# Optimization experiments

Measured on AMD Instinct MI355X. Metric: run time of the kernel, lower is better.

The kernel has to match this reference:

```python
import jax, jax.numpy as jnp
import numpy as np

DELAY_TAPS = np.array([1, 4, 24, 96, 168])
MAX_DELAY = int(DELAY_TAPS.max())
LEAK_RATE = 0.1
RESERVOIR_DIM = 256
INPUT_DIM = 1
N_TAPS = len(DELAY_TAPS)
TARGET_RADIUS = 0.95


def setup_inputs() -> dict:
    key = jax.random.key(0)
    kx, kin, kfb, kb = jax.random.split(key, 4)
    B, T = 64, 2048
    x = jax.random.normal(kx, (B, T, INPUT_DIM), dtype=jnp.float32)
    # W_in ~ U(-0.5, 0.5)
    W_in = jax.random.uniform(kin, (RESERVOIR_DIM, INPUT_DIM), dtype=jnp.float32,
                              minval=-0.5, maxval=0.5)
    # W_fb: sparse gaussian rescaled to ~per-tap spectral radius
    per_tap_radius = TARGET_RADIUS / np.sqrt(N_TAPS)
    kfb1, kfb2 = jax.random.split(kfb)
    W = jax.random.normal(kfb1, (N_TAPS, RESERVOIR_DIM, RESERVOIR_DIM), dtype=jnp.float32)
    mask = jax.random.uniform(kfb2, W.shape) < 0.1
    W = W * mask
    # approx spectral radius of sparse gaussian ~ sqrt(R * density)
    approx_radius = np.sqrt(RESERVOIR_DIM * 0.1)
    W_fb = W * (per_tap_radius / approx_radius)
    tap_weights = jnp.ones((N_TAPS,), dtype=jnp.float32)
    bias = jax.random.uniform(kb, (RESERVOIR_DIM,), dtype=jnp.float32,
                              minval=-0.1, maxval=0.1)
    return {"x": x, "W_in": W_in, "W_fb": W_fb,
            "tap_weights": tap_weights, "bias": bias}


def reference(x, W_in, W_fb, tap_weights, bias):
    B, T, _ = x.shape
    R = W_in.shape[0]
    # static gather positions into rolling history buffer of length MAX_DELAY
    # history[:, -1] holds state at t-1  ->  state at t - tau lives at MAX_DELAY - tau
    pos = MAX_DELAY - DELAY_TAPS  # numpy, static

    drive = jnp.einsum('bti,ri->btr', x, W_in)  # (B,T,R)
    tap_w = jax.nn.softmax(tap_weights)

    h0 = jnp.zeros((B, R), x.dtype)
    hist0 = jnp.zeros((B, MAX_DELAY, R), x.dtype)

    def step(carry, d_t):
        h, hist = carry
        delayed = hist[:, pos, :]  # (B,K,R)
        fb = jnp.einsum('k,bkr,krs->bs', tap_w, delayed, W_fb)
        h_new = (1.0 - LEAK_RATE) * h + LEAK_RATE * jnp.tanh(d_t + fb + bias)
        hist = jnp.concatenate([hist[:, 1:], h_new[:, None, :]], axis=1)
        return (h_new, hist), h_new

    drive_t = jnp.swapaxes(drive, 0, 1)  # (T,B,R)
    _, states = jax.lax.scan(step, (h0, hist0), drive_t)
    return jnp.swapaxes(states, 0, 1)  # (B,T,R)
```

## Files before the change

### kernel.cpp

```cpp
#include <hip/hip_runtime.h>
#include <math.h>

typedef __attribute__((ext_vector_type(8))) short bf16x8;
typedef __attribute__((ext_vector_type(4))) float f32x4;

#define BB 64
#define TT 2048
#define RR 256
#define BLK 24
#define NTHR 512
#define HB_PAD 776
#define HW_PAD 288

#define MFMA(a, b, c) __builtin_amdgcn_mfma_f32_16x16x32_bf16((a), (b), (c), 0, 0, 0)

__device__ __forceinline__ unsigned short f2bf(float f) {
    unsigned u = __float_as_uint(f);
    return (unsigned short)((u + 0x7FFFu + ((u >> 16) & 1u)) >> 16);
}
__device__ __forceinline__ float bf2f(unsigned short h) {
    return __uint_as_float(((unsigned)h) << 16);
}
__device__ __forceinline__ float fast_tanh(float x) {
    float e = __expf(2.0f * x);
    return 1.0f - 2.0f * __builtin_amdgcn_rcpf(1.0f + e);
}

__global__ void pack_weights(const float* __restrict__ W_fb,
                             const float* __restrict__ tapw,
                             unsigned short* __restrict__ bp) {
    int gid = blockIdx.x * 256 + threadIdx.x;
    int l = gid & 63, c = gid >> 6;
    int tap = c >> 7;
    int rem = c & 127;
    int kt = rem >> 4, nt = rem & 15;

    float v0 = tapw[0], v1 = tapw[1], v2 = tapw[2], v3 = tapw[3], v4 = tapw[4];
    float mx = fmaxf(fmaxf(fmaxf(v0, v1), fmaxf(v2, v3)), v4);
    float e0 = expf(v0 - mx), e1 = expf(v1 - mx), e2 = expf(v2 - mx),
          e3 = expf(v3 - mx), e4 = expf(v4 - mx);
    float inv = 1.0f / (e0 + e1 + e2 + e3 + e4);
    float tws[5] = {e0 * inv, e1 * inv, e2 * inv, e3 * inv, e4 * inv};
    float tw = tws[tap];

    int kbase = 32 * kt + 8 * (l >> 4);
    int n = 16 * nt + (l & 15);
    const float* W = W_fb + tap * 65536;
    unsigned short t[8];
#pragma unroll
    for (int j = 0; j < 8; ++j) t[j] = f2bf(tw * W[(kbase + j) * 256 + n]);
    uint4 o;
    o.x = (unsigned)t[0] | ((unsigned)t[1] << 16);
    o.y = (unsigned)t[2] | ((unsigned)t[3] << 16);
    o.z = (unsigned)t[4] | ((unsigned)t[5] << 16);
    o.w = (unsigned)t[6] | ((unsigned)t[7] << 16);
    *(uint4*)(bp + (size_t)(c * 64 + l) * 8) = o;
}

__global__ __launch_bounds__(NTHR, 1)
void reservoir_mfma(const float* __restrict__ x,
                    const float* __restrict__ W_in,
                    const float* __restrict__ bias,
                    const unsigned short* __restrict__ bp,
                    float* __restrict__ out)
{
    const int b    = blockIdx.x;
    const int tid  = threadIdx.x;
    const int lane = tid & 63;
    const int w    = tid >> 6;
    const int l15  = lane & 15;
    const int quad = lane >> 4;

    __shared__ float xs[TT];
    __shared__ unsigned short hwinb[8][2][HW_PAD];
    __shared__ unsigned short hbcb[BLK][2][HB_PAD];
    __shared__ float2 Gl2[BLK][130];
    __shared__ float hob[BLK][RR];

    for (int i = tid; i < TT; i += NTHR) xs[i] = x[b * TT + i];
    {
        unsigned* hz = (unsigned*)&hwinb[0][0][0];
        for (int i = tid; i < 8 * 2 * HW_PAD / 2; i += NTHR) hz[i] = 0u;
    }

    const bf16x8* bpv = (const bf16x8*)bp;
    bf16x8 b1[8][2], b4[8][2];
#pragma unroll
    for (int kt = 0; kt < 8; ++kt)
#pragma unroll
        for (int u = 0; u < 2; ++u) {
            int nt = 2 * w + u;
            b1[kt][u] = bpv[((0 * 8 + kt) * 16 + nt) * 64 + lane];
            b4[kt][u] = bpv[((1 * 8 + kt) * 16 + nt) * 64 + lane];
        }

    const int s0g = 32 * w + l15, s1g = s0g + 16;
    const float win0 = W_in[s0g], win1 = W_in[s1g];
    const float bi0 = bias[s0g], bi1 = bias[s1g];
    float hp0 = 0.0f, hp1 = 0.0f;

    const float* outr = out + (size_t)b * TT * RR;
    float*       outw = out + (size_t)b * TT * RR;

    const unsigned short* hw1v = &hwinb[0][l15 & 1][0];
    const unsigned short* hw4v = &hwinb[0][(l15 >> 2) & 1][0];
    const unsigned short* fa1  = &hbcb[16 + (l15 & 7)][(l15 >> 3) & 1][0];
    const size_t HWSLOT = 2 * HW_PAD;

    const int varw  = quad >> 1;
    const int s_w   = 32 * w + l15 + ((quad & 1) << 4);
    unsigned short* const hwb = &hwinb[0][0][0];
    const unsigned hw_off = (unsigned)(varw * HW_PAD + s_w);

    __syncthreads();

    for (int t0 = 0; t0 < TT; t0 += BLK) {
#pragma unroll
        for (int it = 0; it < 9; ++it) {
            int i = it * NTHR + tid;
            int j = i / 192;
            int p = i - j * 192;
            int r = 4 * p;
            int kf = r >> 8, rr = r & 255;
            float4 v = {0.f, 0.f, 0.f, 0.f};
            if (kf == 0) {
                if (t0 > 0) v = *(const float4*)&hob[j][rr];
            } else {
                int dk = (kf == 1) ? 96 : 168;
                int tt = t0 + j - dk;
                if (tt >= 0) v = *(const float4*)(outr + (size_t)tt * RR + rr);
            }
            unsigned short h0 = f2bf(v.x), h1 = f2bf(v.y), h2 = f2bf(v.z), h3 = f2bf(v.w);
            unsigned short q0 = f2bf(v.x - bf2f(h0)), q1 = f2bf(v.y - bf2f(h1)),
                           q2 = f2bf(v.z - bf2f(h2)), q3 = f2bf(v.w - bf2f(h3));
            uint2 H = { (unsigned)h0 | ((unsigned)h1 << 16), (unsigned)h2 | ((unsigned)h3 << 16) };
            uint2 Q = { (unsigned)q0 | ((unsigned)q1 << 16), (unsigned)q2 | ((unsigned)q3 << 16) };
            *(uint2*)&hbcb[j][0][r] = H;
            *(uint2*)&hbcb[j][1][r] = Q;
        }
        __syncthreads();

        f32x4 zf = {0.f, 0.f, 0.f, 0.f};
        f32x4 cf00a = zf, cf01a = zf, cf00b = zf, cf01b = zf, cf10 = zf, cf11 = zf;
        const int r0a = l15;
        const int cw0 = 2 * w, cw1 = 2 * w + 1;
        bf16x8 p0A = bpv[((16 + 0) * 16 + cw0) * 64 + lane];
        bf16x8 p0B = bpv[((16 + 0) * 16 + cw1) * 64 + lane];
        bf16x8 p1A = bpv[((16 + 1) * 16 + cw0) * 64 + lane];
        bf16x8 p1B = bpv[((16 + 1) * 16 + cw1) * 64 + lane];
        bf16x8 p2A = bpv[((16 + 2) * 16 + cw0) * 64 + lane];
        bf16x8 p2B = bpv[((16 + 2) * 16 + cw1) * 64 + lane];
#pragma unroll 1
        for (int g = 0; g < 8; ++g) {
            const int base = 3 * g;
            {
                int ro = 32 * base + 8 * quad;
                bf16x8 a00 = *(const bf16x8*)&hbcb[r0a][0][ro];
                bf16x8 a01 = *(const bf16x8*)&hbcb[r0a][1][ro];
                bf16x8 a1  = *(const bf16x8*)&fa1[ro];
                cf00a = MFMA(a00, p0A, cf00a); cf01a = MFMA(a00, p0B, cf01a);
                cf00b = MFMA(a01, p0A, cf00b); cf01b = MFMA(a01, p0B, cf01b);
                cf10  = MFMA(a1,  p0A, cf10);  cf11  = MFMA(a1,  p0B, cf11);
                int nf = base + 3; if (nf > 23) nf = 23;
                p0A = bpv[((16 + nf) * 16 + cw0) * 64 + lane];
                p0B = bpv[((16 + nf) * 16 + cw1) * 64 + lane];
            }
            {
                int ro = 32 * (base + 1) + 8 * quad;
                bf16x8 a00 = *(const bf16x8*)&hbcb[r0a][0][ro];
                bf16x8 a01 = *(const bf16x8*)&hbcb[r0a][1][ro];
                bf16x8 a1  = *(const bf16x8*)&fa1[ro];
                cf00a = MFMA(a00, p1A, cf00a); cf01a = MFMA(a00, p1B, cf01a);
                cf00b = MFMA(a01, p1A, cf00b); cf01b = MFMA(a01, p1B, cf01b);
                cf10  = MFMA(a1,  p1A, cf10);  cf11  = MFMA(a1,  p1B, cf11);
                int nf = base + 4; if (nf > 23) nf = 23;
                p1A = bpv[((16 + nf) * 16 + cw0) * 64 + lane];
                p1B = bpv[((16 + nf) * 16 + cw1) * 64 + lane];
            }
            {
                int ro = 32 * (base + 2) + 8 * quad;
                bf16x8 a00 = *(const bf16x8*)&hbcb[r0a][0][ro];
                bf16x8 a01 = *(const bf16x8*)&hbcb[r0a][1][ro];
                bf16x8 a1  = *(const bf16x8*)&fa1[ro];
                cf00a = MFMA(a00, p2A, cf00a); cf01a = MFMA(a00, p2B, cf01a);
                cf00b = MFMA(a01, p2A, cf00b); cf01b = MFMA(a01, p2B, cf01b);
                cf10  = MFMA(a1,  p2A, cf10);  cf11  = MFMA(a1,  p2B, cf11);
                int nf = base + 5; if (nf > 23) nf = 23;
                p2A = bpv[((16 + nf) * 16 + cw0) * 64 + lane];
                p2B = bpv[((16 + nf) * 16 + cw1) * 64 + lane];
            }
        }
        f32x4 cf00 = cf00a + cf00b, cf01 = cf01a + cf01b;
        float cf10f[4], cf11f[4];
#pragma unroll
        for (int i = 0; i < 4; ++i) {
            cf10f[i] = cf10[i] + __shfl_xor(cf10[i], 32, 64);
            cf11f[i] = cf11[i] + __shfl_xor(cf11[i], 32, 64);
        }
#pragma unroll
        for (int i = 0; i < 4; ++i) {
            int j0 = 4 * quad + i;
            int tx0 = t0 + j0; float xv0 = xs[tx0 < TT ? tx0 : TT - 1];
            Gl2[j0][16 * w + l15] =
                make_float2(cf00[i] + bi0 + xv0 * win0, cf01[i] + bi1 + xv0 * win1);
            int j1 = 16 + 4 * quad + i;
            if (j1 < BLK) {
                int tx1 = t0 + j1; float xv1 = xs[tx1 < TT ? tx1 : TT - 1];
                Gl2[j1][16 * w + l15] =
                    make_float2(cf10f[i] + bi0 + xv1 * win0, cf11f[i] + bi1 + xv1 * win1);
            }
        }
        __syncthreads();

        const int tend = (t0 + BLK < TT) ? (t0 + BLK) : TT;
#pragma unroll 1
        for (int t4 = t0; t4 < tend; t4 += 4) {
            f32x4 c40 = zf, c41 = zf;
            const int sl = (t4 - 4 + (l15 & 3)) & 7;
            const unsigned short* hw4 = hw4v + (size_t)sl * HWSLOT;
#pragma unroll
            for (int kt = 0; kt < 8; ++kt) {
                int ro = 32 * kt + 8 * quad;
                bf16x8 a = *(const bf16x8*)&hw4[ro];
                c40 = MFMA(a, b4[kt][0], c40);
                c41 = MFMA(a, b4[kt][1], c41);
            }
            float c40f[4], c41f[4];
#pragma unroll
            for (int u2 = 0; u2 < 4; ++u2) {
                c40f[u2] = c40[u2] + __shfl_xor(c40[u2], 16, 64);
                c41f[u2] = c41[u2] + __shfl_xor(c41[u2], 16, 64);
            }
#pragma unroll
            for (int u = 0; u < 4; ++u) {
                const int t = t4 + u;
                const int sp = (t - 1) & 7;
                const unsigned short* hw1 = hw1v + (size_t)sp * HWSLOT;
                f32x4 c10 = zf, c11 = zf;
#pragma unroll
                for (int kt = 0; kt < 8; ++kt) {
                    int ro = 32 * kt + 8 * quad;
                    bf16x8 a = *(const bf16x8*)&hw1[ro];
                    c10 = MFMA(a, b1[kt][0], c10);
                    c11 = MFMA(a, b1[kt][1], c11);
                }
                const int jj = t - t0;
                const int wsl = t & 7;
                float2 gl = Gl2[jj][16 * w + l15];
                float f0 = (c10[0] + c10[1]) + c40f[u] + gl.x;
                float f1 = (c11[0] + c11[1]) + c41f[u] + gl.y;
                float h0 = 0.9f * hp0 + 0.1f * fast_tanh(f0);
                float h1 = 0.9f * hp1 + 0.1f * fast_tanh(f1);
                hp0 = h0; hp1 = h1;
                unsigned short hh0 = f2bf(h0), hh1 = f2bf(h1);
                unsigned short lo0 = f2bf(h0 - bf2f(hh0)), lo1 = f2bf(h1 - bf2f(hh1));
                unsigned short v0 = varw ? lo0 : hh0;
                unsigned short v1 = varw ? lo1 : hh1;
                unsigned short wv = (quad & 1) ? v1 : v0;
                hwb[(size_t)wsl * HWSLOT + hw_off] = wv;
                if (quad < 2) hob[jj][s_w] = (quad & 1) ? h1 : h0;
                __syncthreads();
            }
        }

        {
            const int nf4 = (tend - t0) * (RR / 4);
            const float4* src = (const float4*)&hob[0][0];
            float4* dst = (float4*)(outw + (size_t)t0 * RR);
#pragma unroll
            for (int it = 0; it < 3; ++it) {
                int idx = it * NTHR + tid;
                if (idx < nf4) dst[idx] = src[idx];
            }
        }
    }
}

extern "C" void kernel_launch(void* const* d_in, const int* in_sizes, int n_in,
                              void* d_out, int out_size, void* d_ws, size_t ws_size,
                              hipStream_t stream) {
    const float* x    = (const float*)d_in[0];
    const float* W_in = (const float*)d_in[1];
    const float* W_fb = (const float*)d_in[2];
    const float* tapw = (const float*)d_in[3];
    const float* bias = (const float*)d_in[4];
    float* out = (float*)d_out;
    unsigned short* bp = (unsigned short*)d_ws;

    pack_weights<<<160, 256, 0, stream>>>(W_fb, tapw, bp);
    reservoir_mfma<<<BB, NTHR, 0, stream>>>(x, W_in, bias, bp, out);
}
```

Before: 1.960 ms.

## Overlap next block's delayed-tap staging and feedback MFMAs with the recurrent step loop

Moves the loading and bf16 hi/lo splitting of the next block's tap-96/168 history rows, along with most of the block-level feedback MFMA accumulation (k-tiles 8..23), into the per-step sequential loop. That work is spread over the step iterations, and the accumulators are carried across blocks. Only the tap-24 rows and the first 8 k-tiles stay in the block prologue. The goal is to hide the serial block-prologue latency behind the latency-bound per-step recurrence, where MFMA and memory units sit idle. The cost is a longer per-step critical path, more register pressure, and timing-sensitive correctness, because staged writes into hbcb must not collide with reads.

```diff
diff --git a/kernel.cpp b/kernel.cpp
--- a/kernel.cpp
+++ b/kernel.cpp
@@ -112,24 +112,28 @@
     unsigned short* const hwb = &hwinb[0][0][0];
     const unsigned hw_off = (unsigned)(varw * HW_PAD + s_w);
 
+    const int r0a = l15;
+    const int cw0 = 2 * w, cw1 = 2 * w + 1;
+    const f32x4 zf = {0.f, 0.f, 0.f, 0.f};
+
+    f32x4 cf00a = zf, cf01a = zf, cf00b = zf, cf01b = zf, cf10 = zf, cf11 = zf;
+    float4 stg = {0.f, 0.f, 0.f, 0.f};
+    int stg_j = 0, stg_r = 256;
+    bf16x8 fpA, fpB;
+
     __syncthreads();
 
     for (int t0 = 0; t0 < TT; t0 += BLK) {
-#pragma unroll
-        for (int it = 0; it < 9; ++it) {
+        bf16x8 qA = bpv[((16 + 0) * 16 + cw0) * 64 + lane];
+        bf16x8 qB = bpv[((16 + 0) * 16 + cw1) * 64 + lane];
+#pragma unroll
+        for (int it = 0; it < 3; ++it) {
             int i = it * NTHR + tid;
-            int j = i / 192;
-            int p = i - j * 192;
+            int j = i >> 6;
+            int p = i & 63;
             int r = 4 * p;
-            int kf = r >> 8, rr = r & 255;
             float4 v = {0.f, 0.f, 0.f, 0.f};
-            if (kf == 0) {
-                if (t0 > 0) v = *(const float4*)&hob[j][rr];
-            } else {
-                int dk = (kf == 1) ? 96 : 168;
-                int tt = t0 + j - dk;
-                if (tt >= 0) v = *(const float4*)(outr + (size_t)tt * RR + rr);
-            }
+            if (t0 > 0) v = *(const float4*)&hob[j][r];
             unsigned short h0 = f2bf(v.x), h1 = f2bf(v.y), h2 = f2bf(v.z), h3 = f2bf(v.w);
             unsigned short q0 = f2bf(v.x - bf2f(h0)), q1 = f2bf(v.y - bf2f(h1)),
                            q2 = f2bf(v.z - bf2f(h2)), q3 = f2bf(v.w - bf2f(h3));
@@ -140,75 +144,42 @@
         }
         __syncthreads();
 
-        f32x4 zf = {0.f, 0.f, 0.f, 0.f};
-        f32x4 cf00a = zf, cf01a = zf, cf00b = zf, cf01b = zf, cf10 = zf, cf11 = zf;
-        const int r0a = l15;
-        const int cw0 = 2 * w, cw1 = 2 * w + 1;
-        bf16x8 p0A = bpv[((16 + 0) * 16 + cw0) * 64 + lane];
-        bf16x8 p0B = bpv[((16 + 0) * 16 + cw1) * 64 + lane];
-        bf16x8 p1A = bpv[((16 + 1) * 16 + cw0) * 64 + lane];
-        bf16x8 p1B = bpv[((16 + 1) * 16 + cw1) * 64 + lane];
-        bf16x8 p2A = bpv[((16 + 2) * 16 + cw0) * 64 + lane];
-        bf16x8 p2B = bpv[((16 + 2) * 16 + cw1) * 64 + lane];
 #pragma unroll 1
-        for (int g = 0; g < 8; ++g) {
-            const int base = 3 * g;
-            {
-                int ro = 32 * base + 8 * quad;
-                bf16x8 a00 = *(const bf16x8*)&hbcb[r0a][0][ro];
-                bf16x8 a01 = *(const bf16x8*)&hbcb[r0a][1][ro];
-                bf16x8 a1  = *(const bf16x8*)&fa1[ro];
-                cf00a = MFMA(a00, p0A, cf00a); cf01a = MFMA(a00, p0B, cf01a);
-                cf00b = MFMA(a01, p0A, cf00b); cf01b = MFMA(a01, p0B, cf01b);
-                cf10  = MFMA(a1,  p0A, cf10);  cf11  = MFMA(a1,  p0B, cf11);
-                int nf = base + 3; if (nf > 23) nf = 23;
-                p0A = bpv[((16 + nf) * 16 + cw0) * 64 + lane];
-                p0B = bpv[((16 + nf) * 16 + cw1) * 64 + lane];
-            }
-            {
-                int ro = 32 * (base + 1) + 8 * quad;
-                bf16x8 a00 = *(const bf16x8*)&hbcb[r0a][0][ro];
-                bf16x8 a01 = *(const bf16x8*)&hbcb[r0a][1][ro];
-                bf16x8 a1  = *(const bf16x8*)&fa1[ro];
-                cf00a = MFMA(a00, p1A, cf00a); cf01a = MFMA(a00, p1B, cf01a);
-                cf00b = MFMA(a01, p1A, cf00b); cf01b = MFMA(a01, p1B, cf01b);
-                cf10  = MFMA(a1,  p1A, cf10);  cf11  = MFMA(a1,  p1B, cf11);
-                int nf = base + 4; if (nf > 23) nf = 23;
-                p1A = bpv[((16 + nf) * 16 + cw0) * 64 + lane];
-                p1B = bpv[((16 + nf) * 16 + cw1) * 64 + lane];
-            }
-            {
-                int ro = 32 * (base + 2) + 8 * quad;
-                bf16x8 a00 = *(const bf16x8*)&hbcb[r0a][0][ro];
-                bf16x8 a01 = *(const bf16x8*)&hbcb[r0a][1][ro];
-                bf16x8 a1  = *(const bf16x8*)&fa1[ro];
-                cf00a = MFMA(a00, p2A, cf00a); cf01a = MFMA(a00, p2B, cf01a);
-                cf00b = MFMA(a01, p2A, cf00b); cf01b = MFMA(a01, p2B, cf01b);
-                cf10  = MFMA(a1,  p2A, cf10);  cf11  = MFMA(a1,  p2B, cf11);
-                int nf = base + 5; if (nf > 23) nf = 23;
-                p2A = bpv[((16 + nf) * 16 + cw0) * 64 + lane];
-                p2B = bpv[((16 + nf) * 16 + cw1) * 64 + lane];
-            }
-        }
-        f32x4 cf00 = cf00a + cf00b, cf01 = cf01a + cf01b;
-        float cf10f[4], cf11f[4];
-#pragma unroll
-        for (int i = 0; i < 4; ++i) {
-            cf10f[i] = cf10[i] + __shfl_xor(cf10[i], 32, 64);
-            cf11f[i] = cf11[i] + __shfl_xor(cf11[i], 32, 64);
-        }
-#pragma unroll
-        for (int i = 0; i < 4; ++i) {
-            int j0 = 4 * quad + i;
-            int tx0 = t0 + j0; float xv0 = xs[tx0 < TT ? tx0 : TT - 1];
-            Gl2[j0][16 * w + l15] =
-                make_float2(cf00[i] + bi0 + xv0 * win0, cf01[i] + bi1 + xv0 * win1);
-            int j1 = 16 + 4 * quad + i;
-            if (j1 < BLK) {
-                int tx1 = t0 + j1; float xv1 = xs[tx1 < TT ? tx1 : TT - 1];
-                Gl2[j1][16 * w + l15] =
-                    make_float2(cf10f[i] + bi0 + xv1 * win0, cf11f[i] + bi1 + xv1 * win1);
-            }
+        for (int ft = 0; ft < 8; ++ft) {
+            bf16x8 B0 = qA, B1 = qB;
+            int nf = (ft < 7) ? ft + 1 : 7;
+            qA = bpv[((16 + nf) * 16 + cw0) * 64 + lane];
+            qB = bpv[((16 + nf) * 16 + cw1) * 64 + lane];
+            int ro = 32 * ft + 8 * quad;
+            bf16x8 a00 = *(const bf16x8*)&hbcb[r0a][0][ro];
+            bf16x8 a01 = *(const bf16x8*)&hbcb[r0a][1][ro];
+            bf16x8 a1  = *(const bf16x8*)&fa1[ro];
+            cf00a = MFMA(a00, B0, cf00a); cf01a = MFMA(a00, B1, cf01a);
+            cf00b = MFMA(a01, B0, cf00b); cf01b = MFMA(a01, B1, cf01b);
+            cf10  = MFMA(a1,  B0, cf10);  cf11  = MFMA(a1,  B1, cf11);
+        }
+        {
+            f32x4 cf00 = cf00a + cf00b, cf01 = cf01a + cf01b;
+            float cf10f[4], cf11f[4];
+#pragma unroll
+            for (int i = 0; i < 4; ++i) {
+                cf10f[i] = cf10[i] + __shfl_xor(cf10[i], 32, 64);
+                cf11f[i] = cf11[i] + __shfl_xor(cf11[i], 32, 64);
+            }
+#pragma unroll
+            for (int i = 0; i < 4; ++i) {
+                int j0 = 4 * quad + i;
+                int tx0 = t0 + j0; float xv0 = xs[tx0 < TT ? tx0 : TT - 1];
+                Gl2[j0][16 * w + l15] =
+                    make_float2(cf00[i] + bi0 + xv0 * win0, cf01[i] + bi1 + xv0 * win1);
+                int j1 = 16 + 4 * quad + i;
+                if (j1 < BLK) {
+                    int tx1 = t0 + j1; float xv1 = xs[tx1 < TT ? tx1 : TT - 1];
+                    Gl2[j1][16 * w + l15] =
+                        make_float2(cf10f[i] + bi0 + xv1 * win0, cf11f[i] + bi1 + xv1 * win1);
+                }
+            }
+            cf00a = zf; cf01a = zf; cf00b = zf; cf01b = zf; cf10 = zf; cf11 = zf;
         }
         __syncthreads();
 
@@ -234,6 +205,7 @@
 #pragma unroll
             for (int u = 0; u < 4; ++u) {
                 const int t = t4 + u;
+                const int jj = t - t0;
                 const int sp = (t - 1) & 7;
                 const unsigned short* hw1 = hw1v + (size_t)sp * HWSLOT;
                 f32x4 c10 = zf, c11 = zf;
@@ -244,14 +216,58 @@
                     c10 = MFMA(a, b1[kt][0], c10);
                     c11 = MFMA(a, b1[kt][1], c11);
                 }
-                const int jj = t - t0;
-                const int wsl = t & 7;
+
+                if (jj >= 1 && jj <= 6) {
+                    unsigned short h0 = f2bf(stg.x), h1 = f2bf(stg.y),
+                                   h2 = f2bf(stg.z), h3 = f2bf(stg.w);
+                    unsigned short q0 = f2bf(stg.x - bf2f(h0)), q1 = f2bf(stg.y - bf2f(h1)),
+                                   q2 = f2bf(stg.z - bf2f(h2)), q3 = f2bf(stg.w - bf2f(h3));
+                    uint2 H = { (unsigned)h0 | ((unsigned)h1 << 16),
+                                (unsigned)h2 | ((unsigned)h3 << 16) };
+                    uint2 Q = { (unsigned)q0 | ((unsigned)q1 << 16),
+                                (unsigned)q2 | ((unsigned)q3 << 16) };
+                    *(uint2*)&hbcb[stg_j][0][stg_r] = H;
+                    *(uint2*)&hbcb[stg_j][1][stg_r] = Q;
+                }
+                if (jj < 6) {
+                    int i2 = jj * NTHR + tid;
+                    stg_j = i2 >> 7;
+                    int p2 = i2 & 127;
+                    stg_r = 256 + 4 * p2;
+                    int kf = stg_r >> 8;
+                    int dk = (kf == 1) ? 96 : 168;
+                    int rr = stg_r & 255;
+                    int tt = t0 + BLK + stg_j - dk;
+                    float4 v = {0.f, 0.f, 0.f, 0.f};
+                    if (tt >= 0) v = *(const float4*)(outr + (size_t)tt * RR + rr);
+                    stg = v;
+                }
+                if (jj == 7) {
+                    fpA = bpv[((16 + 8) * 16 + cw0) * 64 + lane];
+                    fpB = bpv[((16 + 8) * 16 + cw1) * 64 + lane];
+                }
+                if (jj >= 8) {
+                    bf16x8 B0 = fpA, B1 = fpB;
+                    if (jj < 23) {
+                        fpA = bpv[((16 + jj + 1) * 16 + cw0) * 64 + lane];
+                        fpB = bpv[((16 + jj + 1) * 16 + cw1) * 64 + lane];
+                    }
+                    int ro = 32 * jj + 8 * quad;
+                    bf16x8 a00 = *(const bf16x8*)&hbcb[r0a][0][ro];
+                    bf16x8 a01 = *(const bf16x8*)&hbcb[r0a][1][ro];
+                    bf16x8 a1  = *(const bf16x8*)&fa1[ro];
+                    cf00a = MFMA(a00, B0, cf00a); cf01a = MFMA(a00, B1, cf01a);
+                    cf00b = MFMA(a01, B0, cf00b); cf01b = MFMA(a01, B1, cf01b);
+                    cf10  = MFMA(a1,  B0, cf10);  cf11  = MFMA(a1,  B1, cf11);
+                }
+
                 float2 gl = Gl2[jj][16 * w + l15];
                 float f0 = (c10[0] + c10[1]) + c40f[u] + gl.x;
                 float f1 = (c11[0] + c11[1]) + c41f[u] + gl.y;
                 float h0 = 0.9f * hp0 + 0.1f * fast_tanh(f0);
                 float h1 = 0.9f * hp1 + 0.1f * fast_tanh(f1);
                 hp0 = h0; hp1 = h1;
+                const int wsl = t & 7;
                 unsigned short hh0 = f2bf(h0), hh1 = f2bf(h1);
                 unsigned short lo0 = f2bf(h0 - bf2f(hh0)), lo1 = f2bf(h1 - bf2f(hh1));
                 unsigned short v0 = varw ? lo0 : hh0;
```

Result: slower. 2.068 ms (+5.5%).
